# Optimization experiments

Hardware: AMD Instinct MI355X
Metric: run time of the kernel (lower is better)

Reference implementation:

```python
import jax, jax.numpy as jnp
import numpy as np

N_NODES = 10000
N_EDGES = 80000
IN_DIM, HID, OUT_DIM, HEADS = 768, 512, 768, 4
NEG_SLOPE = 0.2


def setup_inputs() -> dict:
    key = jax.random.key(0)
    ks = jax.random.split(key, 10)
    g = 0.05
    return {
        "x": jax.random.normal(ks[0], (N_NODES, IN_DIM), jnp.float32),
        "edge_index": jax.random.randint(ks[1], (2, N_EDGES), 0, N_NODES, jnp.int64),
        # layer 1: GATConv(768 -> 512, heads=4, concat=True)
        "W1": jax.random.normal(ks[2], (IN_DIM, HEADS * HID), jnp.float32) * g,
        "a1_src": jax.random.normal(ks[3], (HEADS, HID), jnp.float32) * g,
        "a1_dst": jax.random.normal(ks[4], (HEADS, HID), jnp.float32) * g,
        "b1": jnp.zeros((HEADS * HID,), jnp.float32),
        # layer 2: GATConv(2048 -> 768, heads=1, concat=False)
        "W2": jax.random.normal(ks[5], (HEADS * HID, OUT_DIM), jnp.float32) * g,
        "a2_src": jax.random.normal(ks[6], (1, OUT_DIM), jnp.float32) * g,
        "a2_dst": jax.random.normal(ks[7], (1, OUT_DIM), jnp.float32) * g,
        "b2": jnp.zeros((OUT_DIM,), jnp.float32),
    }


def _gat_layer(x, src, dst, W, a_src, a_dst, b, heads, d_out, concat):
    N = x.shape[0]
    h = (x @ W).reshape(N, heads, d_out)              # [N, H, D]
    as_n = jnp.einsum('nhd,hd->nh', h, a_src)          # [N, H]
    ad_n = jnp.einsum('nhd,hd->nh', h, a_dst)
    e = jax.nn.leaky_relu(as_n[src] + ad_n[dst], NEG_SLOPE)  # [E, H]
    # segment softmax over destination nodes
    e_max = jax.lax.stop_gradient(jax.ops.segment_max(e, dst, num_segments=N))
    ex = jnp.exp(e - e_max[dst])
    denom = jax.ops.segment_sum(ex, dst, num_segments=N)
    alpha = ex / (denom[dst] + 1e-16)                  # [E, H]
    msg = alpha[:, :, None] * h[src]                   # [E, H, D]
    out = jax.ops.segment_sum(msg, dst, num_segments=N)  # [N, H, D]
    out = out.reshape(N, heads * d_out) if concat else out.mean(axis=1)
    return out + b


def reference(x, edge_index, W1, a1_src, a1_dst, b1, W2, a2_src, a2_dst, b2):
    N = x.shape[0]
    # PyG GATConv default: add self-loops
    loops = jnp.arange(N, dtype=edge_index.dtype)
    src = jnp.concatenate([edge_index[0], loops])
    dst = jnp.concatenate([edge_index[1], loops])
    h = _gat_layer(x, src, dst, W1, a1_src, a1_dst, b1, HEADS, HID, True)
    h = jax.nn.elu(h)
    out = _gat_layer(h, src, dst, W2, a2_src, a2_dst, b2, 1, OUT_DIM, False)
    return out
```

## Files before the change

kernel.cpp:

```cpp
#include <hip/hip_runtime.h>
#include <hip/hip_bf16.h>

#define N_NODES 10000
#define E_REAL  80000
#define E_TOTAL 90000
#define IN_DIM  768
#define HID     512
#define HEADS   4
#define OUT_DIM 768
#define HD1     (HEADS * HID)
#define NEG_SLOPE 0.2f
#define S1_STRIDE (N_NODES * 256)

typedef unsigned short ushort_t;
typedef unsigned int uint_t;

__device__ inline float b2f(ushort_t u) { return __uint_as_float(((uint_t)u) << 16); }
__device__ inline ushort_t f2b(float f) {
    __hip_bfloat16 h = __float2bfloat16(f);
    return *reinterpret_cast<ushort_t*>(&h);
}

__device__ inline void edge_sd(const int* __restrict__ ei, int e, int& s, int& d) {
    if (e < E_REAL) { s = ei[e]; d = ei[E_REAL + e]; }
    else            { s = e - E_REAL; d = s; }
}

#define GLDS(g, l) __builtin_amdgcn_global_load_lds( \
    (const __attribute__((address_space(1))) void*)(g), \
    (__attribute__((address_space(3))) void*)(l), 16, 0, 0)

static const long B_H1B  = 0L;
static const long B_HB   = 40960000L;
static const long B_XB   = 81920000L;
static const long B_W1T  = 97280000L;
static const long B_W2T  = 100425728L;
static const long B_SM   = 103571456L;
static const long SM_AS1   = 0;
static const long SM_AD1   = 40000;
static const long SM_AS2   = 80000;
static const long SM_AD2   = 90000;
static const long SM_CNT   = 100000;
static const long SM_ROWS  = 110000;
static const long SM_CURS  = 120016;
static const long SM_END   = 130016;
static const long B_CSRS = B_SM + SM_END * 4;

__global__ __launch_bounds__(256)
void cast_bf16(const float* __restrict__ in, ushort_t* __restrict__ o, long n) {
    long i = ((long)blockIdx.x * 256 + threadIdx.x) * 8;
    if (i >= n) return;
    float4 v0 = *(const float4*)(in + i);
    float4 v1 = *(const float4*)(in + i + 4);
    ushort_t r[8] = {f2b(v0.x), f2b(v0.y), f2b(v0.z), f2b(v0.w),
                     f2b(v1.x), f2b(v1.y), f2b(v1.z), f2b(v1.w)};
    *(uint4*)(o + i) = *(uint4*)r;
}

__global__ __launch_bounds__(256)
void cast_transpose(const float* __restrict__ W, ushort_t* __restrict__ WT,
                    int K, int N) {
    __shared__ ushort_t t[32][33];
    const int n0 = blockIdx.x * 32, k0 = blockIdx.y * 32;
    const int tx = threadIdx.x & 31, ty = threadIdx.x >> 5;
#pragma unroll
    for (int i = 0; i < 4; ++i) {
        int k = ty + i * 8;
        t[k][tx] = f2b(W[(long)(k0 + k) * N + n0 + tx]);
    }
    __syncthreads();
#pragma unroll
    for (int i = 0; i < 4; ++i) {
        int n = ty + i * 8;
        WT[(long)(n0 + n) * K + k0 + tx] = t[tx][n];
    }
}

typedef short bf16x8 __attribute__((ext_vector_type(8)));
typedef float f32x4 __attribute__((ext_vector_type(4)));

#define GBM 256
#define GBN 128
#define GBK 64
#define ABUF (GBM * GBK)
#define BBUF (GBN * GBK)
#define GEMM_LDS_BYTES ((3 * (ABUF + BBUF)) * 2)

template<int CMODE>
__global__ __launch_bounds__(512)
void gemm8p(const ushort_t* __restrict__ A, const ushort_t* __restrict__ BT,
            ushort_t* __restrict__ C, int M, int N, int K) {
    extern __shared__ ushort_t sm_[];
    ushort_t* smA = sm_;
    ushort_t* smB = sm_ + 3 * ABUF;
    const int tid  = threadIdx.x;
    const int wave = tid >> 6, lane = tid & 63;
    const int quad = lane >> 4, l16 = lane & 15;
    const int bm = blockIdx.y * GBM, bn = blockIdx.x * GBN;
    const int wr = (wave >> 1) * 64, wc = (wave & 1) * 64;
    const int NT = K / GBK;

    const int  rA  = tid >> 3;
    const long cs8 = (long)(((tid & 7) ^ ((tid >> 3) & 7)) * 8);
    const ushort_t* aSrc = A  + (long)(bm + rA) * K + cs8;
    const ushort_t* bSrc = BT + (long)(bn + rA) * K + cs8;

    const int aRd  = (wr + l16) * GBK;
    const int bRd  = (wc + l16) * GBK;
    const int swz8 = l16 & 7;
    const int chq0 = ((quad)     ^ swz8) * 8;
    const int chq1 = ((4 + quad) ^ swz8) * 8;

    f32x4 acc[4][4] = {};

#pragma unroll
    for (int tt = 0; tt < 2; ++tt) {
        const long kt = (long)tt * GBK;
#pragma unroll
        for (int i = 0; i < 4; ++i)
            GLDS(aSrc + (long)i * 64 * K + kt,
                 smA + tt * ABUF + (i * 512 + wave * 64) * 8);
#pragma unroll
        for (int i = 0; i < 2; ++i)
            GLDS(bSrc + (long)i * 64 * K + kt,
                 smB + tt * BBUF + (i * 512 + wave * 64) * 8);
    }
    asm volatile("s_waitcnt vmcnt(6)" ::: "memory");
    __builtin_amdgcn_s_barrier();
    __builtin_amdgcn_sched_barrier(0);

    int bc = 0, bnx = 1, bs = 2;
    for (int t = 0; t < NT; ++t) {
        const int offA = bc * ABUF, offB = bc * BBUF;
        const bool stage = (t + 2 < NT);
        const long kt2 = (long)(t + 2) * GBK;
        bf16x8 bfr[2][4], af[2][2];

#pragma unroll
        for (int j = 0; j < 4; ++j) {
            bfr[0][j] = *(const bf16x8*)(smB + offB + bRd + j * 1024 + chq0);
            bfr[1][j] = *(const bf16x8*)(smB + offB + bRd + j * 1024 + chq1);
        }
#pragma unroll
        for (int ii = 0; ii < 2; ++ii) {
            af[0][ii] = *(const bf16x8*)(smA + offA + aRd + ii * 1024 + chq0);
            af[1][ii] = *(const bf16x8*)(smA + offA + aRd + ii * 1024 + chq1);
        }
        if (stage) {
            GLDS(aSrc + kt2,                    smA + bs * ABUF + (wave * 64) * 8);
            GLDS(aSrc + (long)1 * 64 * K + kt2, smA + bs * ABUF + (512 + wave * 64) * 8);
            GLDS(aSrc + (long)2 * 64 * K + kt2, smA + bs * ABUF + (1024 + wave * 64) * 8);
        }
        __builtin_amdgcn_sched_barrier(0);
        __builtin_amdgcn_s_barrier();
        __builtin_amdgcn_sched_barrier(0);
        __builtin_amdgcn_s_setprio(1);
#pragma unroll
        for (int kk = 0; kk < 2; ++kk)
#pragma unroll
            for (int ii = 0; ii < 2; ++ii)
#pragma unroll
                for (int j = 0; j < 4; ++j)
                    acc[ii][j] = __builtin_amdgcn_mfma_f32_16x16x32_bf16(
                        af[kk][ii], bfr[kk][j], acc[ii][j], 0, 0, 0);
        __builtin_amdgcn_s_setprio(0);
        __builtin_amdgcn_sched_barrier(0);
        __builtin_amdgcn_s_barrier();
        __builtin_amdgcn_sched_barrier(0);

#pragma unroll
        for (int ii = 0; ii < 2; ++ii) {
            af[0][ii] = *(const bf16x8*)(smA + offA + aRd + (2 + ii) * 1024 + chq0);
            af[1][ii] = *(const bf16x8*)(smA + offA + aRd + (2 + ii) * 1024 + chq1);
        }
        if (stage) {
            GLDS(aSrc + (long)3 * 64 * K + kt2, smA + bs * ABUF + (1536 + wave * 64) * 8);
            GLDS(bSrc + kt2,                    smB + bs * BBUF + (wave * 64) * 8);
            GLDS(bSrc + (long)1 * 64 * K + kt2, smB + bs * BBUF + (512 + wave * 64) * 8);
        }
        if (stage)             { asm volatile("s_waitcnt vmcnt(6)" ::: "memory"); }
        else if (t + 1 < NT)   { asm volatile("s_waitcnt vmcnt(0)" ::: "memory"); }
        __builtin_amdgcn_sched_barrier(0);
        __builtin_amdgcn_s_barrier();
        __builtin_amdgcn_sched_barrier(0);
        __builtin_amdgcn_s_setprio(1);
#pragma unroll
        for (int kk = 0; kk < 2; ++kk)
#pragma unroll
            for (int ii = 0; ii < 2; ++ii)
#pragma unroll
                for (int j = 0; j < 4; ++j)
                    acc[2 + ii][j] = __builtin_amdgcn_mfma_f32_16x16x32_bf16(
                        af[kk][ii], bfr[kk][j], acc[2 + ii][j], 0, 0, 0);
        __builtin_amdgcn_s_setprio(0);
        __builtin_amdgcn_sched_barrier(0);
        __builtin_amdgcn_s_barrier();
        __builtin_amdgcn_sched_barrier(0);

        int tmp = bc; bc = bnx; bnx = bs; bs = tmp;
    }

#pragma unroll
    for (int i = 0; i < 4; ++i) {
#pragma unroll
        for (int r = 0; r < 4; ++r) {
            int row = bm + wr + i * 16 + quad * 4 + r;
            if (row >= M) continue;
#pragma unroll
            for (int j = 0; j < 4; ++j) {
                int col = bn + wc + j * 16 + l16;
                if (CMODE == 0) {
                    C[(long)row * N + col] = f2b(acc[i][j][r]);
                } else {
                    C[(long)(col >> 8) * S1_STRIDE + (long)row * 256 + (col & 255)]
                        = f2b(acc[i][j][r]);
                }
            }
        }
    }
}

__global__ __launch_bounds__(256)
void attn1(const ushort_t* __restrict__ h, const float* __restrict__ a_s,
           const float* __restrict__ a_d, float* __restrict__ os,
           float* __restrict__ od) {
    const int n = blockIdx.x;
    const int w = threadIdx.x >> 6, lane = threadIdx.x & 63;
    const int half = lane >> 5, l32 = lane & 31;
    uint4 hv = *(const uint4*)(h + (long)(w * 2 + half) * S1_STRIDE
                                 + (long)n * 256 + l32 * 8);
    const float* asp = a_s + w * HID + half * 256 + l32 * 8;
    const float* adp = a_d + w * HID + half * 256 + l32 * 8;
    const ushort_t* pb = (const ushort_t*)&hv;
    float ps = 0.f, pd = 0.f;
#pragma unroll
    for (int c = 0; c < 8; ++c) {
        float v = b2f(pb[c]);
        ps += v * asp[c];
        pd += v * adp[c];
    }
#pragma unroll
    for (int off = 32; off > 0; off >>= 1) {
        ps += __shfl_down(ps, off);
        pd += __shfl_down(pd, off);
    }
    if (lane == 0) { os[n * HEADS + w] = ps; od[n * HEADS + w] = pd; }
}

__global__ __launch_bounds__(256)
void attn2(const ushort_t* __restrict__ h, const float* __restrict__ a_s,
           const float* __restrict__ a_d, float* __restrict__ os,
           float* __restrict__ od) {
    __shared__ float rs[4], rd[4];
    const int n = blockIdx.x, tid = threadIdx.x;
    const int w = tid >> 6, lane = tid & 63;
    float ps = 0.f, pd = 0.f;
#pragma unroll
    for (int j = 0; j < 3; ++j) {
        int c = tid + j * 256;
        float v = b2f(h[(long)n * OUT_DIM + c]);
        ps += v * a_s[c];
        pd += v * a_d[c];
    }
#pragma unroll
    for (int off = 32; off > 0; off >>= 1) {
        ps += __shfl_down(ps, off);
        pd += __shfl_down(pd, off);
    }
    if (lane == 0) { rs[w] = ps; rd[w] = pd; }
    __syncthreads();
    if (tid == 0) {
        os[n] = rs[0] + rs[1] + rs[2] + rs[3];
        od[n] = rd[0] + rd[1] + rd[2] + rd[3];
    }
}

__global__ __launch_bounds__(256)
void hist_dst(const int* __restrict__ ei, int* __restrict__ cnt) {
    int e = blockIdx.x * 256 + threadIdx.x;
    if (e >= E_TOTAL) return;
    int s, d; edge_sd(ei, e, s, d);
    atomicAdd(&cnt[d], 1);
}

#define SCAN_CH 40
__global__ __launch_bounds__(256)
void scan_nodes(const int* __restrict__ cnt, int* __restrict__ rows,
                int* __restrict__ curs) {
    __shared__ int part[256];
    const int tid = threadIdx.x;
    const int base = tid * SCAN_CH;
    int local[SCAN_CH];
    int sum = 0;
#pragma unroll
    for (int i = 0; i < SCAN_CH; ++i) {
        int idx = base + i;
        int v = (idx < N_NODES) ? cnt[idx] : 0;
        local[i] = v; sum += v;
    }
    part[tid] = sum;
    __syncthreads();
    for (int off = 1; off < 256; off <<= 1) {
        int v = (tid >= off) ? part[tid - off] : 0;
        __syncthreads();
        part[tid] += v;
        __syncthreads();
    }
    int run = part[tid] - sum;
#pragma unroll
    for (int i = 0; i < SCAN_CH; ++i) {
        int idx = base + i;
        if (idx < N_NODES) { rows[idx] = run; curs[idx] = run; run += local[i]; }
    }
    if (tid == 255) rows[N_NODES] = run;
}

__global__ __launch_bounds__(256)
void scatter_edges(const int* __restrict__ ei, int* __restrict__ curs,
                   int* __restrict__ csr_src) {
    int e = blockIdx.x * 256 + threadIdx.x;
    if (e >= E_TOTAL) return;
    int s, d; edge_sd(ei, e, s, d);
    int pos = atomicAdd(&curs[d], 1);
    csr_src[pos] = s;
}

__global__ __launch_bounds__(64)
void agg1(const int* __restrict__ rows, const int* __restrict__ csr_src,
          const float* __restrict__ as_n, const float* __restrict__ ad_n,
          const ushort_t* __restrict__ hf, const float* __restrict__ b1,
          ushort_t* __restrict__ o) {
    const int id = blockIdx.x;
    const int slice = id & 7;
    const int n = id >> 3;
    const int hh = slice >> 1, half = slice & 1;
    const int lane = threadIdx.x;
    const int beg = rows[n], end = rows[n + 1];
    const ushort_t* hsl = hf + (long)slice * S1_STRIDE;
    const float adv = ad_n[(long)n * HEADS + hh];
    float acc[4] = {};
    float dsum = 0.f;
    for (int k = beg; k < end; k += 4) {
        int nk = end - k; if (nk > 4) nk = 4;
        uint2 v[4]; float ex[4];
#pragma unroll
        for (int u = 0; u < 4; ++u) {
            if (u < nk) {
                int s = csr_src[k + u];
                float sc = as_n[(long)s * HEADS + hh] + adv;
                sc = sc > 0.f ? sc : NEG_SLOPE * sc;
                ex[u] = __expf(sc);
                v[u]  = *(const uint2*)(hsl + (long)s * 256 + lane * 4);
            }
        }
#pragma unroll
        for (int u = 0; u < 4; ++u) {
            if (u < nk) {
                dsum += ex[u];
                const ushort_t* p = (const ushort_t*)&v[u];
#pragma unroll
                for (int c = 0; c < 4; ++c) acc[c] += ex[u] * b2f(p[c]);
            }
        }
    }
    const float dinv = 1.f / (dsum + 1e-16f);
    const float* bp = b1 + hh * HID + half * 256 + lane * 4;
    ushort_t r[4];
#pragma unroll
    for (int c = 0; c < 4; ++c) {
        float vv = acc[c] * dinv + bp[c];
        r[c] = f2b(vv > 0.f ? vv : expm1f(vv));
    }
    *(uint2*)(o + (long)n * HD1 + hh * HID + half * 256 + lane * 4) = *(uint2*)r;
}

#define PF2 8
__global__ __launch_bounds__(256)
void agg2(const int* __restrict__ rows, const int* __restrict__ csr_src,
          const float* __restrict__ as_n, const float* __restrict__ ad_n,
          const ushort_t* __restrict__ hf, const float* __restrict__ b2,
          float* __restrict__ out) {
    const int n = blockIdx.x * 4 + (threadIdx.x >> 6);
    const int lane = threadIdx.x & 63;
    const int beg = rows[n], end = rows[n + 1];
    const float adv = ad_n[n];
    float acc[12] = {};
    float dsum = 0.f;
    for (int k = beg; k < end; k += PF2) {
        int nk = end - k; if (nk > PF2) nk = PF2;
        int sv[PF2];
#pragma unroll
        for (int u = 0; u < PF2; ++u)
            if (u < nk) sv[u] = csr_src[k + u];
        uint4 v4[PF2]; uint2 v2[PF2]; float ex[PF2];
#pragma unroll
        for (int u = 0; u < PF2; ++u) {
            if (u < nk) {
                float sc = as_n[sv[u]] + adv;
                sc = sc > 0.f ? sc : NEG_SLOPE * sc;
                ex[u] = __expf(sc);
                const ushort_t* hp = hf + (long)sv[u] * OUT_DIM;
                v4[u] = *(const uint4*)(hp + lane * 8);
                v2[u] = *(const uint2*)(hp + 512 + lane * 4);
            }
        }
#pragma unroll
        for (int u = 0; u < PF2; ++u) {
            if (u < nk) {
                dsum += ex[u];
                const ushort_t* p4 = (const ushort_t*)&v4[u];
                const ushort_t* p2 = (const ushort_t*)&v2[u];
#pragma unroll
                for (int c = 0; c < 8; ++c) acc[c] += ex[u] * b2f(p4[c]);
#pragma unroll
                for (int c = 0; c < 4; ++c) acc[8 + c] += ex[u] * b2f(p2[c]);
            }
        }
    }
    const float dinv = 1.f / (dsum + 1e-16f);
    float* op = out + (long)n * OUT_DIM;
#pragma unroll
    for (int c = 0; c < 8; ++c)
        op[lane * 8 + c] = acc[c] * dinv + b2[lane * 8 + c];
#pragma unroll
    for (int c = 0; c < 4; ++c)
        op[512 + lane * 4 + c] = acc[8 + c] * dinv + b2[512 + lane * 4 + c];
}

extern "C" void kernel_launch(void* const* d_in, const int* in_sizes, int n_in,
                              void* d_out, int out_size, void* d_ws, size_t ws_size,
                              hipStream_t stream) {
    const float* x   = (const float*)d_in[0];
    const int*   ei  = (const int*)d_in[1];
    const float* W1  = (const float*)d_in[2];
    const float* a1s = (const float*)d_in[3];
    const float* a1d = (const float*)d_in[4];
    const float* b1  = (const float*)d_in[5];
    const float* W2  = (const float*)d_in[6];
    const float* a2s = (const float*)d_in[7];
    const float* a2d = (const float*)d_in[8];
    const float* b2  = (const float*)d_in[9];
    float* out = (float*)d_out;
    char* base = (char*)d_ws;

    ushort_t* h1b = (ushort_t*)(base + B_H1B);
    ushort_t* hb  = (ushort_t*)(base + B_HB);
    ushort_t* xb  = (ushort_t*)(base + B_XB);
    ushort_t* h2b = xb;
    ushort_t* w1t = (ushort_t*)(base + B_W1T);
    ushort_t* w2t = (ushort_t*)(base + B_W2T);
    float*    sm  = (float*)(base + B_SM);

    float* as1  = sm + SM_AS1;
    float* ad1  = sm + SM_AD1;
    float* as2  = sm + SM_AS2;
    float* ad2  = sm + SM_AD2;
    int* cnt    = (int*)(sm + SM_CNT);
    int* rows   = (int*)(sm + SM_ROWS);
    int* curs   = (int*)(sm + SM_CURS);
    int* csr_src = (int*)(base + B_CSRS);

    hipMemsetAsync(cnt, 0, 10000 * sizeof(int), stream);

    {
        long nx = (long)N_NODES * IN_DIM;
        cast_bf16<<<(int)(nx / 8 / 256 + 1), 256, 0, stream>>>(x, xb, nx);
        cast_transpose<<<dim3(HD1 / 32, IN_DIM / 32), 256, 0, stream>>>(W1, w1t, IN_DIM, HD1);
        cast_transpose<<<dim3(OUT_DIM / 32, HD1 / 32), 256, 0, stream>>>(W2, w2t, HD1, OUT_DIM);
        hist_dst<<<(E_TOTAL + 255) / 256, 256, 0, stream>>>(ei, cnt);
        scan_nodes<<<1, 256, 0, stream>>>(cnt, rows, curs);
        scatter_edges<<<(E_TOTAL + 255) / 256, 256, 0, stream>>>(ei, curs, csr_src);
    }

    gemm8p<1><<<dim3(HD1 / GBN, (N_NODES + GBM - 1) / GBM), 512, GEMM_LDS_BYTES, stream>>>(
        xb, w1t, h1b, N_NODES, HD1, IN_DIM);
    attn1<<<N_NODES, 256, 0, stream>>>(h1b, a1s, a1d, as1, ad1);
    agg1<<<N_NODES * 8, 64, 0, stream>>>(
        rows, csr_src, as1, ad1, h1b, b1, hb);

    gemm8p<0><<<dim3(OUT_DIM / GBN, (N_NODES + GBM - 1) / GBM), 512, GEMM_LDS_BYTES, stream>>>(
        hb, w2t, h2b, N_NODES, OUT_DIM, HD1);
    attn2<<<N_NODES, 256, 0, stream>>>(h2b, a2s, a2d, as2, ad2);
    agg2<<<N_NODES / 4, 256, 0, stream>>>(
        rows, csr_src, as2, ad2, h2b, b2, out);
}
```

Measured before the change: 333.2 us.

## Precompute per-edge attention exponentials in CSR order before aggregation

```diff
diff --git a/kernel.cpp b/kernel.cpp
--- a/kernel.cpp
+++ b/kernel.cpp
@@ -45,6 +45,9 @@
 static const long SM_CURS  = 120016;
 static const long SM_END   = 130016;
 static const long B_CSRS = B_SM + SM_END * 4;
+static const long B_CSRP = B_CSRS + 360000L;
+static const long B_ALF1 = B_CSRP + 360000L;
+static const long B_ALF2 = B_ALF1 + 1440000L;
 
 __global__ __launch_bounds__(256)
 void cast_bf16(const float* __restrict__ in, ushort_t* __restrict__ o, long n) {
@@ -317,17 +320,51 @@
 
 __global__ __launch_bounds__(256)
 void scatter_edges(const int* __restrict__ ei, int* __restrict__ curs,
-                   int* __restrict__ csr_src) {
+                   int* __restrict__ csr_src, int* __restrict__ csr_pos) {
     int e = blockIdx.x * 256 + threadIdx.x;
     if (e >= E_TOTAL) return;
     int s, d; edge_sd(ei, e, s, d);
     int pos = atomicAdd(&curs[d], 1);
     csr_src[pos] = s;
-}
-
+    csr_pos[e] = pos;
+}
+
+__global__ __launch_bounds__(256)
+void alpha1_k(const int* __restrict__ ei, const int* __restrict__ csr_pos,
+              const float* __restrict__ as_n, const float* __restrict__ ad_n,
+              float* __restrict__ alf) {
+    int e = blockIdx.x * 256 + threadIdx.x;
+    if (e >= E_TOTAL) return;
+    int s, d; edge_sd(ei, e, s, d);
+    float4 av = *(const float4*)(as_n + (long)s * HEADS);
+    float4 dv = *(const float4*)(ad_n + (long)d * HEADS);
+    float sc[4] = {av.x + dv.x, av.y + dv.y, av.z + dv.z, av.w + dv.w};
+    float4 r;
+    float* rp = (float*)&r;
+#pragma unroll
+    for (int h = 0; h < 4; ++h) {
+        float v = sc[h] > 0.f ? sc[h] : NEG_SLOPE * sc[h];
+        rp[h] = __expf(v);
+    }
+    *(float4*)(alf + (long)csr_pos[e] * 4) = r;
+}
+
+__global__ __launch_bounds__(256)
+void alpha2_k(const int* __restrict__ ei, const int* __restrict__ csr_pos,
+              const float* __restrict__ as_n, const float* __restrict__ ad_n,
+              float* __restrict__ alf) {
+    int e = blockIdx.x * 256 + threadIdx.x;
+    if (e >= E_TOTAL) return;
+    int s, d; edge_sd(ei, e, s, d);
+    float sc = as_n[s] + ad_n[d];
+    sc = sc > 0.f ? sc : NEG_SLOPE * sc;
+    alf[csr_pos[e]] = __expf(sc);
+}
+
+#define PF1 8
 __global__ __launch_bounds__(64)
 void agg1(const int* __restrict__ rows, const int* __restrict__ csr_src,
-          const float* __restrict__ as_n, const float* __restrict__ ad_n,
+          const float* __restrict__ alf,
           const ushort_t* __restrict__ hf, const float* __restrict__ b1,
           ushort_t* __restrict__ o) {
     const int id = blockIdx.x;
@@ -337,24 +374,24 @@
     const int lane = threadIdx.x;
     const int beg = rows[n], end = rows[n + 1];
     const ushort_t* hsl = hf + (long)slice * S1_STRIDE;
-    const float adv = ad_n[(long)n * HEADS + hh];
     float acc[4] = {};
     float dsum = 0.f;
-    for (int k = beg; k < end; k += 4) {
-        int nk = end - k; if (nk > 4) nk = 4;
-        uint2 v[4]; float ex[4];
-#pragma unroll
-        for (int u = 0; u < 4; ++u) {
+    for (int k = beg; k < end; k += PF1) {
+        int nk = end - k; if (nk > PF1) nk = PF1;
+        int sv[PF1]; float ex[PF1];
+#pragma unroll
+        for (int u = 0; u < PF1; ++u) {
             if (u < nk) {
-                int s = csr_src[k + u];
-                float sc = as_n[(long)s * HEADS + hh] + adv;
-                sc = sc > 0.f ? sc : NEG_SLOPE * sc;
-                ex[u] = __expf(sc);
-                v[u]  = *(const uint2*)(hsl + (long)s * 256 + lane * 4);
+                sv[u] = csr_src[k + u];
+                ex[u] = alf[(long)(k + u) * 4 + hh];
             }
         }
-#pragma unroll
-        for (int u = 0; u < 4; ++u) {
+        uint2 v[PF1];
+#pragma unroll
+        for (int u = 0; u < PF1; ++u)
+            if (u < nk) v[u] = *(const uint2*)(hsl + (long)sv[u] * 256 + lane * 4);
+#pragma unroll
+        for (int u = 0; u < PF1; ++u) {
             if (u < nk) {
                 dsum += ex[u];
                 const ushort_t* p = (const ushort_t*)&v[u];
@@ -377,28 +414,28 @@
 #define PF2 8
 __global__ __launch_bounds__(256)
 void agg2(const int* __restrict__ rows, const int* __restrict__ csr_src,
-          const float* __restrict__ as_n, const float* __restrict__ ad_n,
+          const float* __restrict__ alf,
           const ushort_t* __restrict__ hf, const float* __restrict__ b2,
           float* __restrict__ out) {
     const int n = blockIdx.x * 4 + (threadIdx.x >> 6);
     const int lane = threadIdx.x & 63;
     const int beg = rows[n], end = rows[n + 1];
-    const float adv = ad_n[n];
     float acc[12] = {};
     float dsum = 0.f;
     for (int k = beg; k < end; k += PF2) {
         int nk = end - k; if (nk > PF2) nk = PF2;
-        int sv[PF2];
-#pragma unroll
-        for (int u = 0; u < PF2; ++u)
-            if (u < nk) sv[u] = csr_src[k + u];
-        uint4 v4[PF2]; uint2 v2[PF2]; float ex[PF2];
+        int sv[PF2]; float ex[PF2];
 #pragma unroll
         for (int u = 0; u < PF2; ++u) {
             if (u < nk) {
-                float sc = as_n[sv[u]] + adv;
-                sc = sc > 0.f ? sc : NEG_SLOPE * sc;
-                ex[u] = __expf(sc);
+                sv[u] = csr_src[k + u];
+                ex[u] = alf[k + u];
+            }
+        }
+        uint4 v4[PF2]; uint2 v2[PF2];
+#pragma unroll
+        for (int u = 0; u < PF2; ++u) {
+            if (u < nk) {
                 const ushort_t* hp = hf + (long)sv[u] * OUT_DIM;
                 v4[u] = *(const uint4*)(hp + lane * 8);
                 v2[u] = *(const uint2*)(hp + 512 + lane * 4);
@@ -459,6 +496,9 @@
     int* rows   = (int*)(sm + SM_ROWS);
     int* curs   = (int*)(sm + SM_CURS);
     int* csr_src = (int*)(base + B_CSRS);
+    int* csr_pos = (int*)(base + B_CSRP);
+    float* alf1  = (float*)(base + B_ALF1);
+    float* alf2  = (float*)(base + B_ALF2);
 
     hipMemsetAsync(cnt, 0, 10000 * sizeof(int), stream);
 
@@ -469,18 +509,20 @@
         cast_transpose<<<dim3(OUT_DIM / 32, HD1 / 32), 256, 0, stream>>>(W2, w2t, HD1, OUT_DIM);
         hist_dst<<<(E_TOTAL + 255) / 256, 256, 0, stream>>>(ei, cnt);
         scan_nodes<<<1, 256, 0, stream>>>(cnt, rows, curs);
-        scatter_edges<<<(E_TOTAL + 255) / 256, 256, 0, stream>>>(ei, curs, csr_src);
+        scatter_edges<<<(E_TOTAL + 255) / 256, 256, 0, stream>>>(ei, curs, csr_src, csr_pos);
     }
 
     gemm8p<1><<<dim3(HD1 / GBN, (N_NODES + GBM - 1) / GBM), 512, GEMM_LDS_BYTES, stream>>>(
         xb, w1t, h1b, N_NODES, HD1, IN_DIM);
     attn1<<<N_NODES, 256, 0, stream>>>(h1b, a1s, a1d, as1, ad1);
+    alpha1_k<<<(E_TOTAL + 255) / 256, 256, 0, stream>>>(ei, csr_pos, as1, ad1, alf1);
     agg1<<<N_NODES * 8, 64, 0, stream>>>(
-        rows, csr_src, as1, ad1, h1b, b1, hb);
+        rows, csr_src, alf1, h1b, b1, hb);
 
     gemm8p<0><<<dim3(OUT_DIM / GBN, (N_NODES + GBM - 1) / GBM), 512, GEMM_LDS_BYTES, stream>>>(
         hb, w2t, h2b, N_NODES, OUT_DIM, HD1);
     attn2<<<N_NODES, 256, 0, stream>>>(h2b, a2s, a2d, as2, ad2);
+    alpha2_k<<<(E_TOTAL + 255) / 256, 256, 0, stream>>>(ei, csr_pos, as2, ad2, alf2);
     agg2<<<N_NODES / 4, 256, 0, stream>>>(
-        rows, csr_src, as2, ad2, h2b, b2, out);
-}
+        rows, csr_src, alf2, h2b, b2, out);
+}
```

After: 349.5 us. 1.05x slower.
